# Performance work log

Hardware: AMD Instinct MI355X
Metric: run time of the kernel (lower is better)

The kernel has to match this reference:

```python
import jax, jax.numpy as jnp
import numpy as np

NUM_NODES = 100000
NUM_EDGES = 3200000
N_PER = 400            # nodes per graph (equal-size graphs)
NUM_GRAPHS = 250
K = 100                # sort-pooling k
DIM = 32
IN_DIM = 128
TOTAL = 3 * DIM + 1    # 97 = concat channel count
GDIM = 128
OUT_DIM = 2
DENSE_DIM = (((K - 2) // 2 + 1) - 5 + 1) * 64  # 46*64 = 2944


def setup_inputs() -> dict:
    key = jax.random.key(0)
    ks = jax.random.split(key, 12)

    def lin(k, shape, fan_in):
        return jax.random.normal(k, shape, jnp.float32) / np.float32(np.sqrt(fan_in))

    return {
        "x": jax.random.normal(ks[0], (NUM_NODES, IN_DIM), jnp.float32),
        "edge_index": jax.random.randint(ks[1], (2, NUM_EDGES), 0, NUM_NODES, dtype=jnp.int32),
        "batch": jnp.arange(NUM_NODES, dtype=jnp.int32) // N_PER,
        "W1": lin(ks[2], (IN_DIM, DIM), IN_DIM), "b1": jnp.zeros((DIM,), jnp.float32),
        "W2": lin(ks[3], (DIM, DIM), DIM),       "b2": jnp.zeros((DIM,), jnp.float32),
        "W3": lin(ks[4], (DIM, DIM), DIM),       "b3": jnp.zeros((DIM,), jnp.float32),
        "W4": lin(ks[5], (DIM, 1), DIM),         "b4": jnp.zeros((1,), jnp.float32),
        "cw1": lin(ks[6], (128, 1, TOTAL), TOTAL),   "cb1": jnp.zeros((128,), jnp.float32),
        "cw2": lin(ks[7], (64, 128, 5), 128 * 5),    "cb2": jnp.zeros((64,), jnp.float32),
        "fw1": lin(ks[8], (GDIM, DENSE_DIM), DENSE_DIM), "fb1": jnp.zeros((GDIM,), jnp.float32),
        "fw3": lin(ks[9], (OUT_DIM, GDIM), GDIM),        "fb3": jnp.zeros((OUT_DIM,), jnp.float32),
    }


def _gcn(h_in, W, b, src, dst, coef, deg_inv):
    # GCNConv (improved=False): D^{-1/2}(A+I)D^{-1/2} (h W) + b
    h = h_in @ W
    agg = jax.ops.segment_sum(h[src] * coef, dst, num_segments=NUM_NODES)
    return agg + h * deg_inv[:, None] + b  # deg_inv = self-loop norm dis[i]^2


def reference(x, edge_index, batch, W1, b1, W2, b2, W3, b3, W4, b4,
              cw1, cb1, cw2, cb2, fw1, fb1, fw3, fb3):
    src, dst = edge_index[0], edge_index[1]
    deg = jax.ops.segment_sum(jnp.ones((NUM_EDGES,), x.dtype), dst, num_segments=NUM_NODES) + 1.0
    dis = jax.lax.rsqrt(deg)
    coef = (dis[src] * dis[dst])[:, None]
    deg_inv = 1.0 / deg

    x1 = jnp.tanh(_gcn(x,  W1, b1, src, dst, coef, deg_inv))
    x2 = jnp.tanh(_gcn(x1, W2, b2, src, dst, coef, deg_inv))
    x3 = jnp.tanh(_gcn(x2, W3, b3, src, dst, coef, deg_inv))
    x4 = jnp.tanh(_gcn(x2, W4, b4, src, dst, coef, deg_inv))  # NB: conv4 consumes x2 (as in source)
    xc = jnp.concatenate([x1, x2, x3, x4], axis=1)  # [N, 97]

    # global_sort_pool: per-graph descending sort by last channel, keep top K nodes
    order = jnp.lexsort((-xc[:, -1], batch))  # primary: graph id, secondary: -last channel
    xs = xc[order].reshape(NUM_GRAPHS, N_PER, TOTAL)[:, :K]  # [B, K, 97]

    # Conv1d(1, 128, kernel=stride=97) over flattened [B,1,K*97] == per-slot linear map
    c1 = jax.nn.relu(jnp.einsum('bkt,ct->bck', xs, cw1[:, 0, :]) + cb1[None, :, None])  # [B,128,K]
    p1 = c1.reshape(NUM_GRAPHS, 128, K // 2, 2).max(axis=-1)  # MaxPool1d(2,2) -> [B,128,50]
    c2 = jax.lax.conv_general_dilated(p1, cw2, (1,), 'VALID',
                                      dimension_numbers=('NCH', 'OIH', 'NCH'))
    c2 = jax.nn.relu(c2 + cb2[None, :, None])  # [B,64,46]

    flat = c2.reshape(NUM_GRAPHS, -1)            # [B, 2944]
    h = jax.nn.relu(flat @ fw1.T + fb1)          # fc1 + relu (dropout = identity in eval)
    logits = h @ fw3.T + fb3                     # fc3
    return jax.nn.log_softmax(logits, axis=-1)
```

## Files before the change

kernel.cpp:

```cpp
#include <hip/hip_runtime.h>
#include <hip/hip_bf16.h>

#define NNODES 100000
#define NEDGES 3200000
#define NPADE  4000000
#define NPER   400
#define NGRAPH 250
#define KTOP   100
#define DIM    32
#define INDIM  128
#define TOTALC 97
#define BSHIFT 7
#define BNODES 128
#define NBUCK  782
#define NCHUNK 200
#define CHSZ   16000

__device__ __forceinline__ float bf(unsigned short u) {
    return __uint_as_float(((unsigned)u) << 16);
}
__device__ __forceinline__ unsigned short f2bf(float f) {
    unsigned u = __float_as_uint(f);
    unsigned r = ((u >> 16) & 1u) + 0x7FFFu;
    return (unsigned short)((u + r) >> 16);
}

#define OW_W1   0
#define OW_B1   4096
#define OW_W2   4128
#define OW_B2   5152
#define OW_W3   5184
#define OW_B3   6208
#define OW_W4   6240
#define OW_B4   6272
#define OW_CW1  6280
#define OW_CB1  18696
#define OW_CW2  18824
#define OW_CB2  59784
#define OW_FW1  59848
#define OW_FB1  436680
#define OW_FW3  436808
#define OW_FB3  437064
#define OW_TOT  437072


__global__ void k_detect(const unsigned int* __restrict__ xw, int* __restrict__ flag) {
    __shared__ int cnt[256];
    int t = threadIdx.x, c = 0;
    for (int i = t; i < 4096; i += 256) {
        unsigned e = (xw[i] >> 23) & 0xFFu;
        if (e >= 100u && e <= 150u) c++;
    }
    cnt[t] = c;
    __syncthreads();
    for (int off = 128; off > 0; off >>= 1) {
        if (t < off) cnt[t] += cnt[t + off];
        __syncthreads();
    }
    if (t == 0) flag[0] = (cnt[0] < 2048) ? 1 : 0;
}

struct Srcs { const void* p[16]; };

__global__ void k_convert(Srcs sr, float* __restrict__ dst, const int* __restrict__ flag) {
    const int st[16] = {OW_W1, OW_B1, OW_W2, OW_B2, OW_W3, OW_B3, OW_W4, OW_B4,
                        OW_CW1, OW_CB1, OW_CW2, OW_CB2, OW_FW1, OW_FB1, OW_FW3, OW_FB3};
    const int nn[16] = {4096, 32, 1024, 32, 1024, 32, 32, 1,
                        12416, 128, 40960, 64, 376832, 128, 256, 2};
    int idx = blockIdx.x * 256 + threadIdx.x;
    if (idx >= OW_TOT) return;
    int isb = flag[0];
    #pragma unroll
    for (int s = 0; s < 16; s++) {
        if (idx >= st[s] && idx < st[s] + nn[s]) {
            int l = idx - st[s];
            dst[idx] = isb ? bf(((const unsigned short*)sr.p[s])[l])
                           : ((const float*)sr.p[s])[l];
        }
    }
}

__global__ void k_wtrans(const float* __restrict__ fw1f, float* __restrict__ fw1t,
                         const float* __restrict__ cw2f, float* __restrict__ w2t8) {
    int i = blockIdx.x * 256 + threadIdx.x;
    if (i < 376832) {
        int j = i / 2944, d = i % 2944;
        fw1t[d * 128 + j] = fw1f[i];
    } else if (i < 376832 + 65536) {
        int k = i - 376832;
        int q = k & 7;
        int co = k >> 3;
        int c = co >> 6, o = co & 63;
        w2t8[k] = (q < 5) ? cw2f[(o * 128 + c) * 5 + q] : 0.f;
    }
}


__global__ __launch_bounds__(1024) void k_hist(const int* __restrict__ ei, int* __restrict__ ghist) {
    __shared__ int h[NBUCK];
    int c = blockIdx.x, t = threadIdx.x;
    for (int i = t; i < NBUCK; i += 1024) h[i] = 0;
    __syncthreads();
    int base = c * CHSZ;
    for (int e = base + t; e < base + CHSZ; e += 1024)
        atomicAdd(&h[ei[NEDGES + e] >> BSHIFT], 1);
    __syncthreads();
    for (int i = t; i < NBUCK; i += 1024) ghist[i * NCHUNK + c] = h[i];
}

__global__ __launch_bounds__(256) void k_scanChunk(int* __restrict__ ghist, int* __restrict__ bcnt) {
    __shared__ int s[256];
    int b = blockIdx.x, t = threadIdx.x;
    int v = (t < NCHUNK) ? ghist[b * NCHUNK + t] : 0;
    s[t] = v;
    __syncthreads();
    for (int o = 1; o < 256; o <<= 1) {
        int u = (t >= o) ? s[t - o] : 0;
        __syncthreads();
        s[t] += u;
        __syncthreads();
    }
    if (t < NCHUNK) ghist[b * NCHUNK + t] = s[t] - v;
    if (t == NCHUNK - 1) bcnt[b] = s[t];
}

__global__ void k_scanB(const int* __restrict__ bcnt, int* __restrict__ boff) {
    __shared__ int s[1024];
    int t = threadIdx.x;
    int v = (t < NBUCK) ? bcnt[t] : 0;
    s[t] = v;
    __syncthreads();
    for (int o = 1; o < 1024; o <<= 1) {
        int u = (t >= o) ? s[t - o] : 0;
        __syncthreads();
        s[t] += u;
        __syncthreads();
    }
    if (t < NBUCK) boff[t] = s[t] - v;
}

__global__ __launch_bounds__(1024) void k_binwrite(const int* __restrict__ ei, const int* __restrict__ boff,
                           const int* __restrict__ ghist, unsigned* __restrict__ staged) {
    __shared__ int cur[NBUCK];
    int c = blockIdx.x, t = threadIdx.x;
    for (int i = t; i < NBUCK; i += 1024) cur[i] = boff[i] + ghist[i * NCHUNK + c];
    __syncthreads();
    int base = c * CHSZ;
    for (int e = base + t; e < base + CHSZ; e += 1024) {
        int s = ei[e], d = ei[NEDGES + e];
        int b = d >> BSHIFT;
        int pos = atomicAdd(&cur[b], 1);
        staged[pos] = ((unsigned)(d & (BNODES - 1)) << 17) | (unsigned)s;
    }
}

__global__ __launch_bounds__(256) void k_nodecnt(const unsigned* __restrict__ staged,
                          const int* __restrict__ boff, int* __restrict__ degi) {
    __shared__ int cnt[BNODES];
    int b = blockIdx.x, t = threadIdx.x;
    if (t < BNODES) cnt[t] = 0;
    __syncthreads();
    int s0 = boff[b];
    int s1 = (b + 1 < NBUCK) ? boff[b + 1] : NEDGES;
    for (int i = s0 + t; i < s1; i += 256)
        atomicAdd(&cnt[staged[i] >> 17], 1);
    __syncthreads();
    int n0 = b << BSHIFT;
    int nn = min(BNODES, NNODES - n0);
    if (t < nn) degi[n0 + t] = cnt[t];
}

__global__ void k_bsum(const int* __restrict__ degi, float* __restrict__ dis,
                       float* __restrict__ dinv, int* __restrict__ bsums) {
    __shared__ int s[256];
    int t = threadIdx.x;
    int i = blockIdx.x * 256 + t;
    int dg = (i < NNODES) ? degi[i] : 0;
    if (i < NNODES) {
        float d = (float)(dg + 1);
        dis[i]  = rsqrtf(d);
        dinv[i] = 1.0f / d;
    }
    s[t] = (i < NNODES) ? ((dg + 7) & ~7) : 0;
    __syncthreads();
    for (int off = 128; off > 0; off >>= 1) {
        if (t < off) s[t] += s[t + off];
        __syncthreads();
    }
    if (t == 0) bsums[blockIdx.x] = s[0];
}

__global__ void k_scanb(int* __restrict__ bsums, int nb) {
    __shared__ int s[512];
    int t = threadIdx.x;
    int v = (t < nb) ? bsums[t] : 0;
    s[t] = v;
    __syncthreads();
    for (int off = 1; off < 512; off <<= 1) {
        int u = (t >= off) ? s[t - off] : 0;
        __syncthreads();
        s[t] += u;
        __syncthreads();
    }
    if (t < nb) bsums[t] = s[t] - v;
}

__global__ void k_scanf(const int* __restrict__ degi, const int* __restrict__ bsums,
                        int* __restrict__ row_off) {
    __shared__ int s[256];
    int t = threadIdx.x;
    int i = blockIdx.x * 256 + t;
    int v = (i < NNODES) ? ((degi[i] + 7) & ~7) : 0;
    s[t] = v;
    __syncthreads();
    for (int off = 1; off < 256; off <<= 1) {
        int u = (t >= off) ? s[t - off] : 0;
        __syncthreads();
        s[t] += u;
        __syncthreads();
    }
    if (i < NNODES) row_off[i] = bsums[blockIdx.x] + s[t] - v;
}

__global__ __launch_bounds__(256) void k_csrfix(const unsigned* __restrict__ staged,
                         const int* __restrict__ boff, const int* __restrict__ row_off,
                         const float* __restrict__ dis,
                         int* __restrict__ csr_src, float* __restrict__ csr_cf) {
    __shared__ int cnt[BNODES];
    __shared__ int rofs[BNODES];
    __shared__ float disl[BNODES];
    int b = blockIdx.x, t = threadIdx.x;
    int n0 = b << BSHIFT;
    int nn = min(BNODES, NNODES - n0);
    if (t < BNODES) {
        cnt[t]  = 0;
        rofs[t] = (t < nn) ? row_off[n0 + t] : 0;
        disl[t] = (t < nn) ? dis[n0 + t] : 0.f;
    }
    __syncthreads();
    int s0 = boff[b];
    int s1 = (b + 1 < NBUCK) ? boff[b + 1] : NEDGES;
    for (int i = s0 + t; i < s1; i += 256) {
        unsigned rec = staged[i];
        int dl = rec >> 17, s = rec & 0x1FFFF;
        int r = atomicAdd(&cnt[dl], 1);
        int slot = rofs[dl] + r;
        csr_src[slot] = s;
        csr_cf[slot]  = dis[s] * disl[dl];
    }
    __syncthreads();
    if (t < nn) {
        int d = cnt[t], dp = (d + 7) & ~7;
        for (int s2 = d; s2 < dp; s2++) {
            csr_src[rofs[t] + s2] = 0;
            csr_cf[rofs[t] + s2]  = 0.f;
        }
    }
}


__global__ void k_mm1(const void* __restrict__ xraw, const float* __restrict__ W1f,
                      const int* __restrict__ flag, float* __restrict__ h) {
    __shared__ float w[INDIM * DIM];
    __shared__ float xsh[8 * INDIM];
    int t = threadIdx.x;
    for (int i = t; i < INDIM * DIM; i += 256) w[i] = W1f[i];
    if (flag[0]) {
        const unsigned int* xsrc = (const unsigned int*)((const unsigned short*)xraw
                                   + (size_t)blockIdx.x * 8 * INDIM);
        for (int i = t; i < 512; i += 256) {
            unsigned u = xsrc[i];
            xsh[2 * i]     = __uint_as_float(u << 16);
            xsh[2 * i + 1] = __uint_as_float(u & 0xFFFF0000u);
        }
    } else {
        const float4* xsrc = (const float4*)((const float*)xraw + (size_t)blockIdx.x * 8 * INDIM);
        float4* xdst = (float4*)xsh;
        for (int i = t; i < 256; i += 256) xdst[i] = xsrc[i];
    }
    __syncthreads();
    int ln = t >> 5, c = t & 31;
    const float* xr = xsh + ln * INDIM;
    float acc = 0.f;
    #pragma unroll 8
    for (int j = 0; j < INDIM; j++) acc += xr[j] * w[j * DIM + c];
    h[(size_t)blockIdx.x * 256 + t] = acc;
}

__global__ void k_gather(const float* __restrict__ xin, const float* __restrict__ h4in,
                         const int* __restrict__ csr_src, const float* __restrict__ csr_cf,
                         const int* __restrict__ row_off, const int* __restrict__ degi,
                         const float* __restrict__ dinv,
                         const float* __restrict__ Wm,
                         const float* __restrict__ bias,
                         const float* __restrict__ w4v,
                         const float* __restrict__ b4,
                         float* __restrict__ xout, float* __restrict__ x4out,
                         float* __restrict__ h4out) {
    __shared__ float wsh[DIM * DIM];
    __shared__ float w4sh[DIM];
    __shared__ float zsh[8 * DIM];
    __shared__ float osh[8 * DIM];
    int t = threadIdx.x;
    if (Wm)  for (int i = t; i < DIM * DIM; i += 256) wsh[i] = Wm[i];
    if (w4v && t < DIM) w4sh[t] = w4v[t];
    int node = blockIdx.x * 8 + (t >> 5);
    int lane = t & 31;
    int wg   = t >> 5;
    int start = row_off[node];
    int cnt   = degi[node];
    int iters = (cnt + 7) >> 3;
    const int4*   ip = (const int4*)(csr_src + start);
    const float4* cp = (const float4*)(csr_cf + start);
    float acc0 = 0.f, acc1 = 0.f;
    if (iters > 0) {
        int4   iA = ip[0], iB = ip[1];
        float4 cA = cp[0], cB = cp[1];
        for (int k = 1; k < iters; k++) {
            int4   nA = ip[2 * k],     nB = ip[2 * k + 1];
            float4 dA = cp[2 * k],     dB = cp[2 * k + 1];
            acc0 += xin[(size_t)iA.x * DIM + lane] * cA.x;
            acc1 += xin[(size_t)iA.y * DIM + lane] * cA.y;
            acc0 += xin[(size_t)iA.z * DIM + lane] * cA.z;
            acc1 += xin[(size_t)iA.w * DIM + lane] * cA.w;
            acc0 += xin[(size_t)iB.x * DIM + lane] * cB.x;
            acc1 += xin[(size_t)iB.y * DIM + lane] * cB.y;
            acc0 += xin[(size_t)iB.z * DIM + lane] * cB.z;
            acc1 += xin[(size_t)iB.w * DIM + lane] * cB.w;
            iA = nA; iB = nB; cA = dA; cB = dB;
        }
        acc0 += xin[(size_t)iA.x * DIM + lane] * cA.x;
        acc1 += xin[(size_t)iA.y * DIM + lane] * cA.y;
        acc0 += xin[(size_t)iA.z * DIM + lane] * cA.z;
        acc1 += xin[(size_t)iA.w * DIM + lane] * cA.w;
        acc0 += xin[(size_t)iB.x * DIM + lane] * cB.x;
        acc1 += xin[(size_t)iB.y * DIM + lane] * cB.y;
        acc0 += xin[(size_t)iB.z * DIM + lane] * cB.z;
        acc1 += xin[(size_t)iB.w * DIM + lane] * cB.w;
    }
    float di = dinv[node];
    float z = acc0 + acc1 + xin[(size_t)node * DIM + lane] * di;
    if (!Wm) {
        xout[(size_t)node * DIM + lane] = tanhf(z + bias[lane]);
    } else {
        zsh[wg * DIM + lane] = z;
        __syncthreads();
        const float* zr = zsh + wg * DIM;
        float a = bias[lane];
        #pragma unroll
        for (int j = 0; j < DIM; j++) a += zr[j] * wsh[j * DIM + lane];
        float outv = tanhf(a);
        xout[(size_t)node * DIM + lane] = outv;
        if (h4out) {
            osh[wg * DIM + lane] = outv;
            __syncthreads();
            if (lane == 0) {
                const float* xr = osh + wg * DIM;
                float a4 = 0.f;
                #pragma unroll
                for (int j = 0; j < DIM; j++) a4 += xr[j] * w4sh[j];
                h4out[node] = a4;
            }
        }
    }
    if (h4in) {
        int cntp = iters << 3;
        float a4 = 0.f;
        for (int ee = lane; ee < cntp; ee += 32)
            a4 += h4in[csr_src[start + ee]] * csr_cf[start + ee];
        for (int off = 16; off > 0; off >>= 1) a4 += __shfl_xor(a4, off, 32);
        if (lane == 0) x4out[node] = tanhf(a4 + h4in[node] * di + b4[0]);
    }
}

__global__ __launch_bounds__(1024) void
k_sortconv1(const float* __restrict__ x1, const float* __restrict__ x2,
            const float* __restrict__ x3, const float* __restrict__ x4,
            const float* __restrict__ cw1f, const float* __restrict__ cb1f,
            float* __restrict__ p1g) {
    __shared__ unsigned long long keys[512];
    __shared__ __align__(16) float xs[32 * 100];
    __shared__ __align__(16) float ws[32 * 128];
    __shared__ int nsh[KTOP];
    int g = blockIdx.x, t = threadIdx.x;
    for (int i = t; i < 512; i += 1024) {
        unsigned long long kk = 0xFFFFFFFFFFFFFFFFULL;
        if (i < NPER) {
            unsigned u = __float_as_uint(x4[g * NPER + i]);
            u = (u & 0x80000000u) ? ~u : (u | 0x80000000u);
            kk = ((unsigned long long)(~u) << 32) | (unsigned)i;
        }
        keys[i] = kk;
    }
    __syncthreads();
    for (int k = 2; k <= 512; k <<= 1)
        for (int j = k >> 1; j > 0; j >>= 1) {
            for (int i = t; i < 512; i += 1024) {
                int l = i ^ j;
                if (l > i) {
                    unsigned long long a = keys[i], b = keys[l];
                    bool asc = ((i & k) == 0);
                    if ((a > b) == asc) { keys[i] = b; keys[l] = a; }
                }
            }
            __syncthreads();
        }
    if (t < KTOP) nsh[t] = g * NPER + (int)(unsigned)(keys[t] & 0xFFFFFFFFu);
    int ct = (t & 31) * 4;
    int kt = (t >> 5) * 4;
    bool act = (t < 800);
    float acc[4][4] = {};
    for (int ch = 0; ch < 3; ch++) {
        const float* arr = (ch == 0) ? x1 : (ch == 1) ? x2 : x3;
        __syncthreads();
        for (int i = t; i < 3200; i += 1024) {
            int q = i & 31, k = i >> 5;
            xs[q * 100 + k] = arr[(size_t)nsh[k] * 32 + q];
        }
        for (int i = t; i < 4096; i += 1024) {
            int c = i & 127, q = i >> 7;
            ws[q * 128 + c] = cw1f[c * TOTALC + ch * 32 + q];
        }
        __syncthreads();
        if (act) {
            for (int q = 0; q < 32; q++) {
                float4 wv = *(const float4*)&ws[q * 128 + ct];
                float4 xv = *(const float4*)&xs[q * 100 + kt];
                float xa[4] = { xv.x, xv.y, xv.z, xv.w };
                float wa[4] = { wv.x, wv.y, wv.z, wv.w };
                #pragma unroll
                for (int a = 0; a < 4; a++)
                    #pragma unroll
                    for (int b = 0; b < 4; b++)
                        acc[a][b] += xa[a] * wa[b];
            }
        }
    }
    if (act) {
        float wa[4];
        #pragma unroll
        for (int b = 0; b < 4; b++) wa[b] = cw1f[(ct + b) * TOTALC + 96];
        #pragma unroll
        for (int a = 0; a < 4; a++) {
            float xv = x4[nsh[kt + a]];
            #pragma unroll
            for (int b = 0; b < 4; b++) acc[a][b] += xv * wa[b];
        }
        int jbase = kt >> 1;
        #pragma unroll
        for (int b = 0; b < 4; b++) {
            float bias = cb1f[ct + b];
            float m0 = fmaxf(fmaxf(acc[0][b], acc[1][b]) + bias, 0.f);
            float m1 = fmaxf(fmaxf(acc[2][b], acc[3][b]) + bias, 0.f);
            p1g[((size_t)g * 128 + ct + b) * 50 + jbase]     = m0;
            p1g[((size_t)g * 128 + ct + b) * 50 + jbase + 1] = m1;
        }
    }
}

__global__ __launch_bounds__(512) void
k_conv2(const float* __restrict__ p1g, const float* __restrict__ w2t8,
        const float* __restrict__ cb2f, float* __restrict__ flatg) {
    __shared__ __align__(16) float p1s[128 * 52];
    __shared__ float fl[64 * 25];
    int bid = blockIdx.x;
    int g = bid >> 1, ph = bid & 1;
    int t = threadIdx.x;
    int p0 = ph ? 24 : 0;
    int np = ph ? 22 : 24;
    for (int i = t; i < 128 * 50; i += 512) {
        int c = i / 50, p = i % 50;
        p1s[c * 52 + p] = p1g[(size_t)g * 6400 + i];
    }
    for (int i = t; i < 128 * 2; i += 512) {
        int c = i >> 1;
        p1s[c * 52 + 50 + (i & 1)] = 0.f;
    }
    for (int i = t; i < 64 * 25; i += 512) fl[i] = 0.f;
    __syncthreads();
    {
        int o = t & 63;
        int c8 = t >> 6;
        float acc[24];
        #pragma unroll
        for (int p = 0; p < 24; p++) acc[p] = 0.f;
        int cbeg = c8 * 16;
        for (int c = cbeg; c < cbeg + 16; c++) {
            const float4* wb = (const float4*)(w2t8 + (((size_t)c * 64 + o) << 3));
            float4 wA = wb[0], wB = wb[1];
            float w0 = wA.x, w1 = wA.y, w2 = wA.z, w3 = wA.w, w4 = wB.x;
            float win[28];
            const float4* wsrc = (const float4*)&p1s[c * 52 + p0];
            #pragma unroll
            for (int v = 0; v < 7; v++) {
                float4 f = wsrc[v];
                win[4 * v] = f.x; win[4 * v + 1] = f.y; win[4 * v + 2] = f.z; win[4 * v + 3] = f.w;
            }
            #pragma unroll
            for (int p = 0; p < 24; p++)
                acc[p] += win[p] * w0 + win[p + 1] * w1 + win[p + 2] * w2
                        + win[p + 3] * w3 + win[p + 4] * w4;
        }
        for (int p = 0; p < np; p++) atomicAdd(&fl[o * 25 + p], acc[p]);
    }
    __syncthreads();
    for (int i = t; i < 64 * 24; i += 512) {
        int o = i / 24, p = i - o * 24;
        if (p < np)
            flatg[(size_t)g * 2944 + o * 46 + p0 + p] = fmaxf(fl[o * 25 + p] + cb2f[o], 0.f);
    }
}

__global__ __launch_bounds__(1024) void
k_fc1(const float* __restrict__ flatg, const float* __restrict__ fw1t,
      float* __restrict__ hpart) {
    __shared__ float fls[5 * 368];
    __shared__ float hp[8 * 5 * 128];
    int b = blockIdx.x;
    int gt = b >> 3, kt = b & 7;
    int t = threadIdx.x;
    int g0 = gt * 5;
    int d0 = kt * 368;
    for (int i = t; i < 5 * 368; i += 1024) {
        int g = i / 368, dd = i - g * 368;
        fls[i] = flatg[(size_t)(g0 + g) * 2944 + d0 + dd];
    }
    __syncthreads();
    int og = t & 127, s8 = t >> 7;
    int ds = s8 * 46;
    const float* wp = fw1t + (size_t)(d0 + ds) * 128 + og;
    const float* f0 = fls + ds;
    float a0 = 0.f, a1 = 0.f, a2 = 0.f, a3 = 0.f, a4 = 0.f;
    #pragma unroll 2
    for (int d = 0; d < 46; d++) {
        float w = wp[(size_t)d * 128];
        a0 += f0[d]            * w;
        a1 += f0[368 + d]      * w;
        a2 += f0[2 * 368 + d]  * w;
        a3 += f0[3 * 368 + d]  * w;
        a4 += f0[4 * 368 + d]  * w;
    }
    hp[(s8 * 5 + 0) * 128 + og] = a0;
    hp[(s8 * 5 + 1) * 128 + og] = a1;
    hp[(s8 * 5 + 2) * 128 + og] = a2;
    hp[(s8 * 5 + 3) * 128 + og] = a3;
    hp[(s8 * 5 + 4) * 128 + og] = a4;
    __syncthreads();
    if (t < 640) {
        int g = t >> 7, o2 = t & 127;
        float s = 0.f;
        #pragma unroll
        for (int s2 = 0; s2 < 8; s2++) s += hp[(s2 * 5 + g) * 128 + o2];
        hpart[((size_t)kt * NGRAPH + g0 + g) * 128 + o2] = s;
    }
}

__global__ void k_fc3(const float* __restrict__ hpart, const float* __restrict__ fb1f,
                      const float* __restrict__ fw3f, const float* __restrict__ fb3f,
                      const int* __restrict__ flag, void* __restrict__ outp) {
    __shared__ float hsh[128];
    int g = blockIdx.x, t = threadIdx.x;
    float s = fb1f[t];
    #pragma unroll
    for (int kt = 0; kt < 8; kt++) s += hpart[((size_t)kt * NGRAPH + g) * 128 + t];
    hsh[t] = fmaxf(s, 0.f);
    __syncthreads();
    if (t < 64) {
        float h0 = hsh[t], h1 = hsh[t + 64];
        float l0 = h0 * fw3f[t] + h1 * fw3f[t + 64];
        float l1 = h0 * fw3f[128 + t] + h1 * fw3f[192 + t];
        #pragma unroll
        for (int off = 32; off > 0; off >>= 1) {
            l0 += __shfl_down(l0, off, 64);
            l1 += __shfl_down(l1, off, 64);
        }
        if (t == 0) {
            l0 += fb3f[0]; l1 += fb3f[1];
            float m = fmaxf(l0, l1);
            float lse = m + logf(expf(l0 - m) + expf(l1 - m));
            if (flag[0]) {
                unsigned short* ob = (unsigned short*)outp;
                ob[g * 2 + 0] = f2bf(l0 - lse);
                ob[g * 2 + 1] = f2bf(l1 - lse);
            } else {
                float* of = (float*)outp;
                of[g * 2 + 0] = l0 - lse;
                of[g * 2 + 1] = l1 - lse;
            }
        }
    }
}


extern "C" void kernel_launch(void* const* d_in, const int* in_sizes, int n_in,
                              void* d_out, int out_size, void* d_ws, size_t ws_size,
                              hipStream_t stream) {
    const void* x  = d_in[0];
    const int* ei  = (const int*)d_in[1];

    char* p = (char*)d_ws;
    auto alloc = [&](size_t bytes) -> void* {
        void* r = (void*)p;
        p += (bytes + 255) & ~(size_t)255;
        return r;
    };
    int*      flag    = (int*)alloc(256);
    float*    wcv     = (float*)alloc((size_t)OW_TOT * 4);
    float*    fw1t    = (float*)alloc((size_t)376832 * 4);
    int*      ghist   = (int*)alloc((size_t)NBUCK * NCHUNK * 4);
    int*      bcnt    = (int*)alloc(1024 * 4);
    int*      boff    = (int*)alloc(1024 * 4);
    int*      bsums   = (int*)alloc(512 * 4);
    int*      degi    = (int*)alloc((size_t)NNODES * 4);
    int*      row_off = (int*)alloc((size_t)NNODES * 4);
    float*    dis     = (float*)alloc((size_t)NNODES * 4);
    float*    dinv    = (float*)alloc((size_t)NNODES * 4);
    unsigned* staged  = (unsigned*)alloc((size_t)NEDGES * 4);
    int*      csr_src = (int*)alloc((size_t)NPADE * 4);
    float*    csr_cf  = (float*)alloc((size_t)NPADE * 4);
    float*    hbuf    = (float*)alloc((size_t)NNODES * DIM * 4);
    float*    h4buf   = (float*)alloc((size_t)NNODES * 4);
    float*    x1      = (float*)alloc((size_t)NNODES * DIM * 4);
    float*    x2      = (float*)alloc((size_t)NNODES * DIM * 4);
    float*    x3      = (float*)alloc((size_t)NNODES * DIM * 4);
    float*    x4      = (float*)alloc((size_t)NNODES * 4);
    float*    p1g     = (float*)alloc((size_t)NGRAPH * 128 * 50 * 4);
    float*    w2t     = (float*)alloc((size_t)64 * 128 * 8 * 4);
    float*    flatg   = (float*)alloc((size_t)NGRAPH * 2944 * 4);
    float*    hpart   = (float*)alloc((size_t)8 * NGRAPH * 128 * 4);
    (void)in_sizes; (void)n_in; (void)out_size; (void)ws_size;

    k_detect<<<1, 256, 0, stream>>>((const unsigned int*)x, flag);
    Srcs sr;
    for (int i = 0; i < 16; i++) sr.p[i] = d_in[3 + i];
    k_convert<<<(OW_TOT + 255) / 256, 256, 0, stream>>>(sr, wcv, flag);
    k_wtrans <<<1728, 256, 0, stream>>>(wcv + OW_FW1, fw1t, wcv + OW_CW2, w2t);

    k_hist     <<<NCHUNK, 1024, 0, stream>>>(ei, ghist);
    k_scanChunk<<<NBUCK, 256, 0, stream>>>(ghist, bcnt);
    k_scanB    <<<1, 1024, 0, stream>>>(bcnt, boff);
    k_binwrite <<<NCHUNK, 1024, 0, stream>>>(ei, boff, ghist, staged);
    k_nodecnt  <<<NBUCK, 256, 0, stream>>>(staged, boff, degi);
    k_bsum     <<<391, 256, 0, stream>>>(degi, dis, dinv, bsums);
    k_scanb    <<<1, 512, 0, stream>>>(bsums, 391);
    k_scanf    <<<391, 256, 0, stream>>>(degi, bsums, row_off);
    k_csrfix   <<<NBUCK, 256, 0, stream>>>(staged, boff, row_off, dis, csr_src, csr_cf);

    k_mm1   <<<12500, 256, 0, stream>>>(x, wcv + OW_W1, flag, hbuf);
    k_gather<<<12500, 256, 0, stream>>>(hbuf, nullptr, csr_src, csr_cf, row_off, degi, dinv,
                                        nullptr, wcv + OW_B1, nullptr, nullptr,
                                        x1, nullptr, nullptr);
    k_gather<<<12500, 256, 0, stream>>>(x1, nullptr, csr_src, csr_cf, row_off, degi, dinv,
                                        wcv + OW_W2, wcv + OW_B2, wcv + OW_W4, nullptr,
                                        x2, nullptr, h4buf);
    k_gather<<<12500, 256, 0, stream>>>(x2, h4buf, csr_src, csr_cf, row_off, degi, dinv,
                                        wcv + OW_W3, wcv + OW_B3, nullptr, wcv + OW_B4,
                                        x3, x4, nullptr);

    k_sortconv1<<<NGRAPH, 1024, 0, stream>>>(x1, x2, x3, x4, wcv + OW_CW1, wcv + OW_CB1, p1g);
    k_conv2    <<<2 * NGRAPH, 512, 0, stream>>>(p1g, w2t, wcv + OW_CB2, flatg);
    k_fc1      <<<400, 1024, 0, stream>>>(flatg, fw1t, hpart);
    k_fc3      <<<NGRAPH, 128, 0, stream>>>(hpart, wcv + OW_FB1, wcv + OW_FW3, wcv + OW_FB3,
                                            flag, d_out);
}
```

Baseline: 576.1 us.

## Merge setup kernels, fuse CSR build into cooperative kernel, fuse fc1 with fc3

Detect, convert and weight-transpose are merged into one setup kernel that reads the source weights directly. The nine CSR-construction kernels become one cooperative kernel of 200 blocks that uses grid.sync between phases, with the old multi-kernel path kept as a fallback if the cooperative launch fails. fc3 is folded into fc1: the last-arriving block per graph tile, found with an atomic counter, does the final reduction and log-softmax. The aim is to cut kernel launch and tail overhead, at the cost of grid-wide barriers and lower parallelism in some phases, for example single-block scans and the 200-block CSR fix pass.

```diff
diff --git a/kernel.cpp b/kernel.cpp
--- a/kernel.cpp
+++ b/kernel.cpp
@@ -1,5 +1,8 @@
 #include <hip/hip_runtime.h>
 #include <hip/hip_bf16.h>
+#include <hip/hip_cooperative_groups.h>
+
+namespace cg = cooperative_groups;
 
 #define NNODES 100000
 #define NEDGES 3200000
@@ -15,6 +18,7 @@
 #define NBUCK  782
 #define NCHUNK 200
 #define CHSZ   16000
+#define NTILE  98
 
 __device__ __forceinline__ float bf(unsigned short u) {
     return __uint_as_float(((unsigned)u) << 16);
@@ -43,58 +47,218 @@
 #define OW_FB3  437064
 #define OW_TOT  437072
 
-
-__global__ void k_detect(const unsigned int* __restrict__ xw, int* __restrict__ flag) {
-    __shared__ int cnt[256];
-    int t = threadIdx.x, c = 0;
+struct Srcs { const void* p[16]; };
+
+__global__ void k_setup(const unsigned int* __restrict__ xw, Srcs sr,
+                        float* __restrict__ dst, float* __restrict__ fw1t,
+                        float* __restrict__ w2t8, int* __restrict__ flag,
+                        int* __restrict__ fcnt) {
+    __shared__ int cs[256];
+    int t = threadIdx.x;
+    int c = 0;
     for (int i = t; i < 4096; i += 256) {
         unsigned e = (xw[i] >> 23) & 0xFFu;
         if (e >= 100u && e <= 150u) c++;
     }
-    cnt[t] = c;
+    cs[t] = c;
     __syncthreads();
     for (int off = 128; off > 0; off >>= 1) {
-        if (t < off) cnt[t] += cnt[t + off];
-        __syncthreads();
-    }
-    if (t == 0) flag[0] = (cnt[0] < 2048) ? 1 : 0;
-}
-
-struct Srcs { const void* p[16]; };
-
-__global__ void k_convert(Srcs sr, float* __restrict__ dst, const int* __restrict__ flag) {
-    const int st[16] = {OW_W1, OW_B1, OW_W2, OW_B2, OW_W3, OW_B3, OW_W4, OW_B4,
-                        OW_CW1, OW_CB1, OW_CW2, OW_CB2, OW_FW1, OW_FB1, OW_FW3, OW_FB3};
-    const int nn[16] = {4096, 32, 1024, 32, 1024, 32, 32, 1,
-                        12416, 128, 40960, 64, 376832, 128, 256, 2};
-    int idx = blockIdx.x * 256 + threadIdx.x;
-    if (idx >= OW_TOT) return;
-    int isb = flag[0];
-    #pragma unroll
-    for (int s = 0; s < 16; s++) {
-        if (idx >= st[s] && idx < st[s] + nn[s]) {
-            int l = idx - st[s];
-            dst[idx] = isb ? bf(((const unsigned short*)sr.p[s])[l])
-                           : ((const float*)sr.p[s])[l];
-        }
-    }
-}
-
-__global__ void k_wtrans(const float* __restrict__ fw1f, float* __restrict__ fw1t,
-                         const float* __restrict__ cw2f, float* __restrict__ w2t8) {
-    int i = blockIdx.x * 256 + threadIdx.x;
-    if (i < 376832) {
-        int j = i / 2944, d = i % 2944;
-        fw1t[d * 128 + j] = fw1f[i];
-    } else if (i < 376832 + 65536) {
-        int k = i - 376832;
+        if (t < off) cs[t] += cs[t + off];
+        __syncthreads();
+    }
+    int isb = (cs[0] < 2048) ? 1 : 0;
+    if (blockIdx.x == 0) {
+        if (t == 0) flag[0] = isb;
+        if (t < 64) fcnt[t] = 0;
+    }
+    long idx = (long)blockIdx.x * 256 + t;
+    if (idx < OW_TOT) {
+        const int st[16] = {OW_W1, OW_B1, OW_W2, OW_B2, OW_W3, OW_B3, OW_W4, OW_B4,
+                            OW_CW1, OW_CB1, OW_CW2, OW_CB2, OW_FW1, OW_FB1, OW_FW3, OW_FB3};
+        const int nn[16] = {4096, 32, 1024, 32, 1024, 32, 32, 1,
+                            12416, 128, 40960, 64, 376832, 128, 256, 2};
+        #pragma unroll
+        for (int s = 0; s < 16; s++) {
+            if (idx >= st[s] && idx < st[s] + nn[s]) {
+                int l = (int)idx - st[s];
+                dst[idx] = isb ? bf(((const unsigned short*)sr.p[s])[l])
+                               : ((const float*)sr.p[s])[l];
+            }
+        }
+    } else if (idx < OW_TOT + 376832) {
+        int i2 = (int)(idx - OW_TOT);
+        float v = isb ? bf(((const unsigned short*)sr.p[12])[i2])
+                      : ((const float*)sr.p[12])[i2];
+        int j = i2 / 2944, d = i2 - j * 2944;
+        fw1t[d * 128 + j] = v;
+    } else if (idx < OW_TOT + 376832 + 65536) {
+        int k = (int)(idx - OW_TOT - 376832);
         int q = k & 7;
         int co = k >> 3;
-        int c = co >> 6, o = co & 63;
-        w2t8[k] = (q < 5) ? cw2f[(o * 128 + c) * 5 + q] : 0.f;
-    }
-}
-
+        int cc = co >> 6, o = co & 63;
+        float v = 0.f;
+        if (q < 5) {
+            int si = (o * 128 + cc) * 5 + q;
+            v = isb ? bf(((const unsigned short*)sr.p[10])[si])
+                    : ((const float*)sr.p[10])[si];
+        }
+        w2t8[k] = v;
+    }
+}
+
+__global__ __launch_bounds__(1024) void
+k_prep(const int* __restrict__ ei, int* __restrict__ ghist, int* __restrict__ bcnt,
+       int* __restrict__ boff, unsigned* __restrict__ staged, int* __restrict__ degi,
+       float* __restrict__ dis, float* __restrict__ dinv, int* __restrict__ bsums,
+       int* __restrict__ row_off, int* __restrict__ csr_src, float* __restrict__ csr_cf) {
+    cg::grid_group grid = cg::this_grid();
+    __shared__ int shA[NBUCK];
+    __shared__ int shS[1024];
+    __shared__ int shc[BNODES];
+    __shared__ int shr[BNODES];
+    __shared__ float shd[BNODES];
+    int blk = blockIdx.x, t = threadIdx.x;
+
+    {
+        for (int i = t; i < NBUCK; i += 1024) shA[i] = 0;
+        __syncthreads();
+        int base = blk * CHSZ;
+        for (int e = base + t; e < base + CHSZ; e += 1024)
+            atomicAdd(&shA[ei[NEDGES + e] >> BSHIFT], 1);
+        __syncthreads();
+        for (int i = t; i < NBUCK; i += 1024) ghist[i * NCHUNK + blk] = shA[i];
+    }
+    grid.sync();
+    for (int b = blk; b < NBUCK; b += 200) {
+        int v = (t < NCHUNK) ? ghist[b * NCHUNK + t] : 0;
+        shS[t] = v;
+        __syncthreads();
+        for (int o = 1; o < 1024; o <<= 1) {
+            int u = (t >= o) ? shS[t - o] : 0;
+            __syncthreads();
+            shS[t] += u;
+            __syncthreads();
+        }
+        if (t < NCHUNK) ghist[b * NCHUNK + t] = shS[t] - v;
+        if (t == NCHUNK - 1) bcnt[b] = shS[t];
+        __syncthreads();
+    }
+    grid.sync();
+    if (blk == 0) {
+        int v = (t < NBUCK) ? bcnt[t] : 0;
+        shS[t] = v;
+        __syncthreads();
+        for (int o = 1; o < 1024; o <<= 1) {
+            int u = (t >= o) ? shS[t - o] : 0;
+            __syncthreads();
+            shS[t] += u;
+            __syncthreads();
+        }
+        if (t < NBUCK) boff[t] = shS[t] - v;
+    }
+    grid.sync();
+    {
+        for (int i = t; i < NBUCK; i += 1024) shA[i] = boff[i] + ghist[i * NCHUNK + blk];
+        __syncthreads();
+        int base = blk * CHSZ;
+        for (int e = base + t; e < base + CHSZ; e += 1024) {
+            int s = ei[e], d = ei[NEDGES + e];
+            int b = d >> BSHIFT;
+            int pos = atomicAdd(&shA[b], 1);
+            staged[pos] = ((unsigned)(d & (BNODES - 1)) << 17) | (unsigned)s;
+        }
+    }
+    grid.sync();
+    for (int b = blk; b < NBUCK; b += 200) {
+        if (t < BNODES) shc[t] = 0;
+        __syncthreads();
+        int s0 = boff[b];
+        int s1 = (b + 1 < NBUCK) ? boff[b + 1] : NEDGES;
+        for (int i = s0 + t; i < s1; i += 1024)
+            atomicAdd(&shc[staged[i] >> 17], 1);
+        __syncthreads();
+        int n0 = b << BSHIFT;
+        int nn = min(BNODES, NNODES - n0);
+        if (t < nn) degi[n0 + t] = shc[t];
+        __syncthreads();
+    }
+    grid.sync();
+    for (int tile = blk; tile < NTILE; tile += 200) {
+        int i = tile * 1024 + t;
+        int dg = (i < NNODES) ? degi[i] : 0;
+        if (i < NNODES) {
+            float d = (float)(dg + 1);
+            dis[i]  = rsqrtf(d);
+            dinv[i] = 1.0f / d;
+        }
+        shS[t] = (i < NNODES) ? ((dg + 7) & ~7) : 0;
+        __syncthreads();
+        for (int off = 512; off > 0; off >>= 1) {
+            if (t < off) shS[t] += shS[t + off];
+            __syncthreads();
+        }
+        if (t == 0) bsums[tile] = shS[0];
+        __syncthreads();
+    }
+    grid.sync();
+    if (blk == 0) {
+        int v = (t < NTILE) ? bsums[t] : 0;
+        shS[t] = v;
+        __syncthreads();
+        for (int o = 1; o < 1024; o <<= 1) {
+            int u = (t >= o) ? shS[t - o] : 0;
+            __syncthreads();
+            shS[t] += u;
+            __syncthreads();
+        }
+        if (t < NTILE) bsums[t] = shS[t] - v;
+    }
+    grid.sync();
+    for (int tile = blk; tile < NTILE; tile += 200) {
+        int i = tile * 1024 + t;
+        int v = (i < NNODES) ? ((degi[i] + 7) & ~7) : 0;
+        shS[t] = v;
+        __syncthreads();
+        for (int o = 1; o < 1024; o <<= 1) {
+            int u = (t >= o) ? shS[t - o] : 0;
+            __syncthreads();
+            shS[t] += u;
+            __syncthreads();
+        }
+        if (i < NNODES) row_off[i] = bsums[tile] + shS[t] - v;
+        __syncthreads();
+    }
+    grid.sync();
+    for (int b = blk; b < NBUCK; b += 200) {
+        int n0 = b << BSHIFT;
+        int nn = min(BNODES, NNODES - n0);
+        if (t < BNODES) {
+            shc[t] = 0;
+            shr[t] = (t < nn) ? row_off[n0 + t] : 0;
+            shd[t] = (t < nn) ? dis[n0 + t] : 0.f;
+        }
+        __syncthreads();
+        int s0 = boff[b];
+        int s1 = (b + 1 < NBUCK) ? boff[b + 1] : NEDGES;
+        for (int i = s0 + t; i < s1; i += 1024) {
+            unsigned rec = staged[i];
+            int dl = rec >> 17, s = rec & 0x1FFFF;
+            int r = atomicAdd(&shc[dl], 1);
+            int slot = shr[dl] + r;
+            csr_src[slot] = s;
+            csr_cf[slot]  = dis[s] * shd[dl];
+        }
+        __syncthreads();
+        if (t < nn) {
+            int d = shc[t], dp = (d + 7) & ~7;
+            for (int s2 = d; s2 < dp; s2++) {
+                csr_src[shr[t] + s2] = 0;
+                csr_cf[shr[t] + s2]  = 0.f;
+            }
+        }
+        __syncthreads();
+    }
+}
 
 __global__ __launch_bounds__(1024) void k_hist(const int* __restrict__ ei, int* __restrict__ ghist) {
     __shared__ int h[NBUCK];
@@ -512,10 +676,15 @@
 }
 
 __global__ __launch_bounds__(1024) void
-k_fc1(const float* __restrict__ flatg, const float* __restrict__ fw1t,
-      float* __restrict__ hpart) {
+k_fc1fc3(const float* __restrict__ flatg, const float* __restrict__ fw1t,
+         float* __restrict__ hpart, int* __restrict__ fcnt,
+         const float* __restrict__ fb1f, const float* __restrict__ fw3f,
+         const float* __restrict__ fb3f, const int* __restrict__ flag,
+         void* __restrict__ outp) {
     __shared__ float fls[5 * 368];
     __shared__ float hp[8 * 5 * 128];
+    __shared__ float hsh2[5 * 128];
+    __shared__ int lastf;
     int b = blockIdx.x;
     int gt = b >> 3, kt = b & 7;
     int t = threadIdx.x;
@@ -553,39 +722,48 @@
         for (int s2 = 0; s2 < 8; s2++) s += hp[(s2 * 5 + g) * 128 + o2];
         hpart[((size_t)kt * NGRAPH + g0 + g) * 128 + o2] = s;
     }
-}
-
-__global__ void k_fc3(const float* __restrict__ hpart, const float* __restrict__ fb1f,
-                      const float* __restrict__ fw3f, const float* __restrict__ fb3f,
-                      const int* __restrict__ flag, void* __restrict__ outp) {
-    __shared__ float hsh[128];
-    int g = blockIdx.x, t = threadIdx.x;
-    float s = fb1f[t];
-    #pragma unroll
-    for (int kt = 0; kt < 8; kt++) s += hpart[((size_t)kt * NGRAPH + g) * 128 + t];
-    hsh[t] = fmaxf(s, 0.f);
-    __syncthreads();
-    if (t < 64) {
-        float h0 = hsh[t], h1 = hsh[t + 64];
-        float l0 = h0 * fw3f[t] + h1 * fw3f[t + 64];
-        float l1 = h0 * fw3f[128 + t] + h1 * fw3f[192 + t];
+    __syncthreads();
+    if (t == 0) {
+        __threadfence();
+        int old = atomicAdd(&fcnt[gt], 1);
+        lastf = (old == 7);
+        if (old == 7) atomicExch(&fcnt[gt], 0);
+    }
+    __syncthreads();
+    if (!lastf) return;
+    __threadfence();
+    int gg2 = t >> 7, tt = t & 127;
+    if (t < 640) {
+        int gid = g0 + gg2;
+        float s = fb1f[tt];
+        #pragma unroll
+        for (int k2 = 0; k2 < 8; k2++)
+            s += hpart[((size_t)k2 * NGRAPH + gid) * 128 + tt];
+        hsh2[gg2 * 128 + tt] = fmaxf(s, 0.f);
+    }
+    __syncthreads();
+    if (t < 640 && tt < 64) {
+        float h0 = hsh2[gg2 * 128 + tt], h1 = hsh2[gg2 * 128 + tt + 64];
+        float l0 = h0 * fw3f[tt] + h1 * fw3f[tt + 64];
+        float l1 = h0 * fw3f[128 + tt] + h1 * fw3f[192 + tt];
         #pragma unroll
         for (int off = 32; off > 0; off >>= 1) {
             l0 += __shfl_down(l0, off, 64);
             l1 += __shfl_down(l1, off, 64);
         }
-        if (t == 0) {
+        if (tt == 0) {
+            int gid = g0 + gg2;
             l0 += fb3f[0]; l1 += fb3f[1];
             float m = fmaxf(l0, l1);
             float lse = m + logf(expf(l0 - m) + expf(l1 - m));
             if (flag[0]) {
                 unsigned short* ob = (unsigned short*)outp;
-                ob[g * 2 + 0] = f2bf(l0 - lse);
-                ob[g * 2 + 1] = f2bf(l1 - lse);
+                ob[gid * 2 + 0] = f2bf(l0 - lse);
+                ob[gid * 2 + 1] = f2bf(l1 - lse);
             } else {
                 float* of = (float*)outp;
-                of[g * 2 + 0] = l0 - lse;
-                of[g * 2 + 1] = l1 - lse;
+                of[gid * 2 + 0] = l0 - lse;
+                of[gid * 2 + 1] = l1 - lse;
             }
         }
     }
@@ -605,6 +783,7 @@
         return r;
     };
     int*      flag    = (int*)alloc(256);
+    int*      fcnt    = (int*)alloc(256);
     float*    wcv     = (float*)alloc((size_t)OW_TOT * 4);
     float*    fw1t    = (float*)alloc((size_t)376832 * 4);
     int*      ghist   = (int*)alloc((size_t)NBUCK * NCHUNK * 4);
@@ -630,21 +809,28 @@
     float*    hpart   = (float*)alloc((size_t)8 * NGRAPH * 128 * 4);
     (void)in_sizes; (void)n_in; (void)out_size; (void)ws_size;
 
-    k_detect<<<1, 256, 0, stream>>>((const unsigned int*)x, flag);
     Srcs sr;
     for (int i = 0; i < 16; i++) sr.p[i] = d_in[3 + i];
-    k_convert<<<(OW_TOT + 255) / 256, 256, 0, stream>>>(sr, wcv, flag);
-    k_wtrans <<<1728, 256, 0, stream>>>(wcv + OW_FW1, fw1t, wcv + OW_CW2, w2t);
-
-    k_hist     <<<NCHUNK, 1024, 0, stream>>>(ei, ghist);
-    k_scanChunk<<<NBUCK, 256, 0, stream>>>(ghist, bcnt);
-    k_scanB    <<<1, 1024, 0, stream>>>(bcnt, boff);
-    k_binwrite <<<NCHUNK, 1024, 0, stream>>>(ei, boff, ghist, staged);
-    k_nodecnt  <<<NBUCK, 256, 0, stream>>>(staged, boff, degi);
-    k_bsum     <<<391, 256, 0, stream>>>(degi, dis, dinv, bsums);
-    k_scanb    <<<1, 512, 0, stream>>>(bsums, 391);
-    k_scanf    <<<391, 256, 0, stream>>>(degi, bsums, row_off);
-    k_csrfix   <<<NBUCK, 256, 0, stream>>>(staged, boff, row_off, dis, csr_src, csr_cf);
+    k_setup<<<3436, 256, 0, stream>>>((const unsigned int*)x, sr, wcv, fw1t, w2t, flag, fcnt);
+
+    {
+        void* args[12] = { (void*)&ei, (void*)&ghist, (void*)&bcnt, (void*)&boff,
+                           (void*)&staged, (void*)&degi, (void*)&dis, (void*)&dinv,
+                           (void*)&bsums, (void*)&row_off, (void*)&csr_src, (void*)&csr_cf };
+        hipError_t ce = hipLaunchCooperativeKernel((void*)k_prep, dim3(200), dim3(1024),
+                                                   args, 0, stream);
+        if (ce != hipSuccess) {
+            k_hist     <<<NCHUNK, 1024, 0, stream>>>(ei, ghist);
+            k_scanChunk<<<NBUCK, 256, 0, stream>>>(ghist, bcnt);
+            k_scanB    <<<1, 1024, 0, stream>>>(bcnt, boff);
+            k_binwrite <<<NCHUNK, 1024, 0, stream>>>(ei, boff, ghist, staged);
+            k_nodecnt  <<<NBUCK, 256, 0, stream>>>(staged, boff, degi);
+            k_bsum     <<<391, 256, 0, stream>>>(degi, dis, dinv, bsums);
+            k_scanb    <<<1, 512, 0, stream>>>(bsums, 391);
+            k_scanf    <<<391, 256, 0, stream>>>(degi, bsums, row_off);
+            k_csrfix   <<<NBUCK, 256, 0, stream>>>(staged, boff, row_off, dis, csr_src, csr_cf);
+        }
+    }
 
     k_mm1   <<<12500, 256, 0, stream>>>(x, wcv + OW_W1, flag, hbuf);
     k_gather<<<12500, 256, 0, stream>>>(hbuf, nullptr, csr_src, csr_cf, row_off, degi, dinv,
@@ -659,7 +845,6 @@
 
     k_sortconv1<<<NGRAPH, 1024, 0, stream>>>(x1, x2, x3, x4, wcv + OW_CW1, wcv + OW_CB1, p1g);
     k_conv2    <<<2 * NGRAPH, 512, 0, stream>>>(p1g, w2t, wcv + OW_CB2, flatg);
-    k_fc1      <<<400, 1024, 0, stream>>>(flatg, fw1t, hpart);
-    k_fc3      <<<NGRAPH, 128, 0, stream>>>(hpart, wcv + OW_FB1, wcv + OW_FW3, wcv + OW_FB3,
-                                            flag, d_out);
-}
+    k_fc1fc3   <<<400, 1024, 0, stream>>>(flatg, fw1t, hpart, fcnt, wcv + OW_FB1,
+                                          wcv + OW_FW3, wcv + OW_FB3, flag, d_out);
+}
```

Result: slower. 821.4 us (+42.6%).
